# Performance work log

Measured on AMD Instinct MI355X. Metric: run time of the kernel, lower is better.

The kernel has to match this reference:

```python
import jax, jax.numpy as jnp
import numpy as np

B, L, K, D, H = 2048, 1024, 128, 64, 4


def setup_inputs() -> dict:
    key = jax.random.key(0)
    ks = jax.random.split(key, 16)
    s = 1.0 / np.sqrt(D).astype(np.float32)  # keep softmax unsaturated
    return {
        "indices": jax.random.randint(ks[0], (B, K), 0, L),
        "user_seq_emb": jax.random.normal(ks[1], (B, L, D), jnp.float32),
        "target_emb": jax.random.normal(ks[2], (B, 1, D), jnp.float32),
        "WQ": jax.random.normal(ks[3], (H, D, D), jnp.float32) * s,
        "bQ": jax.random.normal(ks[4], (H, D), jnp.float32) * s,
        "WK": jax.random.normal(ks[5], (H, D, D), jnp.float32) * s,
        "bK": jax.random.normal(ks[6], (H, D), jnp.float32) * s,
        "WV": jax.random.normal(ks[7], (H, D, D), jnp.float32) * s,
        "bV": jax.random.normal(ks[8], (H, D), jnp.float32) * s,
        "WO": jax.random.normal(ks[9], (H * D, D), jnp.float32) * s,
        "bO": jax.random.normal(ks[10], (D,), jnp.float32) * s,
        "W1": jax.random.normal(ks[11], (2 * D, D), jnp.float32) * s,
        "b1": jax.random.normal(ks[12], (D,), jnp.float32) * s,
        "W2": jax.random.normal(ks[13], (D, 1), jnp.float32) * s,
        "b2": jax.random.normal(ks[14], (1,), jnp.float32) * s,
    }


def reference(indices, user_seq_emb, target_emb, WQ, bQ, WK, bK, WV, bV,
              WO, bO, W1, b1, W2, b2):
    d = user_seq_emb.shape[-1]
    # gather top-K history items: [B, K, D]
    topk = jnp.take_along_axis(user_seq_emb, indices[:, :, None], axis=1)
    # per-head projections, vectorized over heads (original loops in Python)
    q = jnp.einsum("bod,hde->bhoe", target_emb, WQ) + bQ[None, :, None, :]  # [B,H,1,D]
    k = jnp.einsum("bkd,hde->bhke", topk, WK) + bK[None, :, None, :]        # [B,H,K,D]
    v = jnp.einsum("bkd,hde->bhke", topk, WV) + bV[None, :, None, :]        # [B,H,K,D]
    scores = jnp.einsum("bhoe,bhke->bhk", q, k) / np.sqrt(d).astype(np.float32)
    attn = jax.nn.softmax(scores, axis=-1)                                   # [B,H,K]
    heads = jnp.einsum("bhk,bhke->bhe", attn, v)                             # [B,H,D]
    mhta = heads.reshape(heads.shape[0], -1) @ WO + bO                       # [B,D]
    # prediction layer: concat with target, MLP -> logit
    x = jnp.concatenate([mhta, target_emb[:, 0, :]], axis=-1)                # [B,2D]
    h = jax.nn.relu(x @ W1 + b1)
    logit = h @ W2 + b2                                                      # [B,1]
    return logit
```

## Files before the change

### kernel.cpp

```cpp
#include <hip/hip_runtime.h>
#include <hip/hip_bf16.h>

#define BB 2048
#define LL 1024
#define KK 128
#define DD 64
#define HH 4

__global__ __launch_bounds__(256) void prep_kernel(
    const float* __restrict__ tgt, const float* __restrict__ WQ,
    const float* __restrict__ bQ, const float* __restrict__ WK,
    const float* __restrict__ bK, float* __restrict__ wkq_out,
    float* __restrict__ sb_out)
{
    __shared__ float sT[8][64];
    __shared__ float sQ[8][256];
    const int t = threadIdx.x;
    const int h = t >> 6, e = t & 63;
    const float myBQ = bQ[t];
    const float myBK = bK[t];
    for (int g = 0; g < 2; g++) {
        const int b0 = (blockIdx.x * 2 + g) * 8;
        for (int i = t; i < 512; i += 256)
            sT[i >> 6][i & 63] = tgt[(size_t)(b0 + (i >> 6)) * 64 + (i & 63)];
        __syncthreads();
        float acc[8];
        #pragma unroll
        for (int j = 0; j < 8; j++) acc[j] = myBQ;
        for (int d = 0; d < 64; d++) {
            float w = WQ[((h << 6) + d) * 64 + e];
            #pragma unroll
            for (int j = 0; j < 8; j++) acc[j] += sT[j][d] * w;
        }
        #pragma unroll
        for (int j = 0; j < 8; j++) sQ[j][t] = acc[j];
        __syncthreads();
        #pragma unroll
        for (int j = 0; j < 8; j++) {
            float p = acc[j] * myBK;
            #pragma unroll
            for (int o = 32; o > 0; o >>= 1) p += __shfl_xor(p, o);
            if (e == 0) sb_out[(b0 + j) * 4 + h] = p * 0.125f;
        }
        float acc2[8];
        #pragma unroll
        for (int j = 0; j < 8; j++) acc2[j] = 0.f;
        const float* wrow = WK + (size_t)t * 64;
        for (int i = 0; i < 64; i += 4) {
            float4 w4 = *(const float4*)(wrow + i);
            #pragma unroll
            for (int j = 0; j < 8; j++) {
                acc2[j] += w4.x * sQ[j][(h << 6) + i]
                         + w4.y * sQ[j][(h << 6) + i + 1]
                         + w4.z * sQ[j][(h << 6) + i + 2]
                         + w4.w * sQ[j][(h << 6) + i + 3];
            }
        }
        #pragma unroll
        for (int j = 0; j < 8; j++)
            wkq_out[(size_t)(b0 + j) * 256 + t] = acc2[j] * 0.125f;
        __syncthreads();
    }
}

__global__ __launch_bounds__(256) void attn_kernel(
    const int* __restrict__ idx, const float* __restrict__ seq,
    const float* __restrict__ wkq_in, const float* __restrict__ sb_in,
    float* __restrict__ ctx_out)
{
    __shared__ float sTop[KK * 65];
    __shared__ float sWkq[256];
    __shared__ float sSb[HH];
    __shared__ float sSc[HH * KK];
    __shared__ float sAt[HH * KK];
    __shared__ int sIdx[KK];
    const int t = threadIdx.x;
    const int b = blockIdx.x;
    if (t < KK) sIdx[t] = idx[b * KK + t];
    sWkq[t] = wkq_in[(size_t)b * 256 + t];
    if (t < HH) sSb[t] = sb_in[b * HH + t];
    __syncthreads();
    for (int i = t; i < 2048; i += 256) {
        int row = i >> 4, c0 = (i & 15) * 4;
        float4 v = *(const float4*)(seq + ((size_t)b * LL + sIdx[row]) * DD + c0);
        float* dst = &sTop[row * 65 + c0];
        dst[0] = v.x; dst[1] = v.y; dst[2] = v.z; dst[3] = v.w;
    }
    __syncthreads();
    #pragma unroll
    for (int s = 0; s < 2; s++) {
        int id = (s << 8) + t;
        int h = id >> 7, k = id & 127;
        float acc = 0.f;
        #pragma unroll
        for (int d = 0; d < DD; d++)
            acc += sTop[k * 65 + d] * sWkq[(h << 6) + d];
        sSc[(h << 7) + k] = acc + sSb[h];
    }
    __syncthreads();
    const int w = t >> 6, lane = t & 63;
    float x0 = sSc[(w << 7) + lane], x1 = sSc[(w << 7) + 64 + lane];
    float m = fmaxf(x0, x1);
    #pragma unroll
    for (int o = 32; o > 0; o >>= 1) m = fmaxf(m, __shfl_xor(m, o));
    float e0 = __expf(x0 - m), e1 = __expf(x1 - m);
    float s = e0 + e1;
    #pragma unroll
    for (int o = 32; o > 0; o >>= 1) s += __shfl_xor(s, o);
    float inv = 1.f / s;
    sAt[(w << 7) + lane] = e0 * inv;
    sAt[(w << 7) + 64 + lane] = e1 * inv;
    __syncthreads();
    float acc = 0.f;
    #pragma unroll 8
    for (int k = 0; k < KK; k++)
        acc += sAt[(w << 7) + k] * sTop[k * 65 + lane];
    ctx_out[(size_t)b * 256 + t] = acc;
}

__global__ __launch_bounds__(256) void out_kernel(
    const float* __restrict__ ctx_in, const float* __restrict__ tgt,
    const float* __restrict__ WV, const float* __restrict__ bV,
    const float* __restrict__ WO, const float* __restrict__ bO,
    const float* __restrict__ W1, const float* __restrict__ b1,
    const float* __restrict__ W2, const float* __restrict__ b2,
    float* __restrict__ outp)
{
    __shared__ float sCtx[8][256];
    __shared__ float sH[8][256];
    __shared__ float sP[8][256];
    __shared__ float sX[8][128];
    const int t = threadIdx.x;
    const int h = t >> 6, e = t & 63;
    const float myBV = bV[t];
    for (int g = 0; g < 2; g++) {
        const int b0 = (blockIdx.x * 2 + g) * 8;
        #pragma unroll
        for (int j = 0; j < 8; j++)
            sCtx[j][t] = ctx_in[(size_t)(b0 + j) * 256 + t];
        for (int i = t; i < 512; i += 256)
            sX[i >> 6][64 + (i & 63)] = tgt[(size_t)(b0 + (i >> 6)) * 64 + (i & 63)];
        __syncthreads();
        float acc[8];
        #pragma unroll
        for (int j = 0; j < 8; j++) acc[j] = myBV;
        for (int d = 0; d < 64; d++) {
            float w = WV[((h << 6) + d) * 64 + e];
            #pragma unroll
            for (int j = 0; j < 8; j++) acc[j] += sCtx[j][(h << 6) + d] * w;
        }
        #pragma unroll
        for (int j = 0; j < 8; j++) sH[j][t] = acc[j];
        __syncthreads();
        float pa[8];
        #pragma unroll
        for (int j = 0; j < 8; j++) pa[j] = 0.f;
        for (int i = 0; i < 64; i++) {
            float w = WO[((h << 6) + i) * 64 + e];
            #pragma unroll
            for (int j = 0; j < 8; j++) pa[j] += sH[j][(h << 6) + i] * w;
        }
        #pragma unroll
        for (int j = 0; j < 8; j++) sP[j][t] = pa[j];
        __syncthreads();
        #pragma unroll
        for (int s = 0; s < 2; s++) {
            int id = (s << 8) + t;
            int j = id >> 6, ee = id & 63;
            sX[j][ee] = sP[j][ee] + sP[j][64 + ee] + sP[j][128 + ee]
                      + sP[j][192 + ee] + bO[ee];
        }
        __syncthreads();
        #pragma unroll
        for (int s = 0; s < 2; s++) {
            int j = (s << 2) + (t >> 6);
            int n = t & 63;
            float a1 = b1[n];
            #pragma unroll 4
            for (int i = 0; i < 128; i++)
                a1 += sX[j][i] * W1[i * 64 + n];
            a1 = fmaxf(a1, 0.f);
            float p = a1 * W2[n];
            #pragma unroll
            for (int o = 32; o > 0; o >>= 1) p += __shfl_xor(p, o);
            if (n == 0) outp[b0 + j] = p + b2[0];
        }
        __syncthreads();
    }
}

extern "C" void kernel_launch(void* const* d_in, const int* in_sizes, int n_in,
                              void* d_out, int out_size, void* d_ws, size_t ws_size,
                              hipStream_t stream)
{
    const int*   idx = (const int*)d_in[0];
    const float* seq = (const float*)d_in[1];
    const float* tgt = (const float*)d_in[2];
    const float* WQ  = (const float*)d_in[3];
    const float* bQ  = (const float*)d_in[4];
    const float* WK  = (const float*)d_in[5];
    const float* bK  = (const float*)d_in[6];
    const float* WV  = (const float*)d_in[7];
    const float* bV  = (const float*)d_in[8];
    const float* WO  = (const float*)d_in[9];
    const float* bO  = (const float*)d_in[10];
    const float* W1  = (const float*)d_in[11];
    const float* b1  = (const float*)d_in[12];
    const float* W2  = (const float*)d_in[13];
    const float* b2  = (const float*)d_in[14];

    float* wkq = (float*)d_ws;
    float* sb  = wkq + (size_t)BB * 256;
    float* ctx = sb + (size_t)BB * 4;
    float* outp = (float*)d_out;

    prep_kernel<<<dim3(BB / 16), dim3(256), 0, stream>>>(tgt, WQ, bQ, WK, bK, wkq, sb);
    attn_kernel<<<dim3(BB), dim3(256), 0, stream>>>(idx, seq, wkq, sb, ctx);
    out_kernel<<<dim3(BB / 16), dim3(256), 0, stream>>>(ctx, tgt, WV, bV, WO, bO,
                                                        W1, b1, W2, b2, outp);
}
```

Baseline: 713.9 us.

## Fuse prep, attention and output MLP into one per-batch kernel

Merges the three kernels into a single kernel with one block per batch row, so the workspace round-trips for wkq, sb and ctx and two launches go away. The gather loads for the top-K rows are issued into registers before the Q/WK projection is computed, letting the gather latency overlap that math. In exchange, the weight matrices are re-read per batch row instead of being amortised over 8 rows per block, which raises L2/cache traffic and per-block serial work.

```diff
diff --git a/kernel.cpp b/kernel.cpp
--- a/kernel.cpp
+++ b/kernel.cpp
@@ -1,5 +1,4 @@
 #include <hip/hip_runtime.h>
-#include <hip/hip_bf16.h>
 
 #define BB 2048
 #define LL 1024
@@ -7,185 +6,153 @@
 #define DD 64
 #define HH 4
 
-__global__ __launch_bounds__(256) void prep_kernel(
-    const float* __restrict__ tgt, const float* __restrict__ WQ,
-    const float* __restrict__ bQ, const float* __restrict__ WK,
-    const float* __restrict__ bK, float* __restrict__ wkq_out,
-    float* __restrict__ sb_out)
-{
-    __shared__ float sT[8][64];
-    __shared__ float sQ[8][256];
-    const int t = threadIdx.x;
-    const int h = t >> 6, e = t & 63;
-    const float myBQ = bQ[t];
-    const float myBK = bK[t];
-    for (int g = 0; g < 2; g++) {
-        const int b0 = (blockIdx.x * 2 + g) * 8;
-        for (int i = t; i < 512; i += 256)
-            sT[i >> 6][i & 63] = tgt[(size_t)(b0 + (i >> 6)) * 64 + (i & 63)];
-        __syncthreads();
-        float acc[8];
-        #pragma unroll
-        for (int j = 0; j < 8; j++) acc[j] = myBQ;
-        for (int d = 0; d < 64; d++) {
-            float w = WQ[((h << 6) + d) * 64 + e];
-            #pragma unroll
-            for (int j = 0; j < 8; j++) acc[j] += sT[j][d] * w;
-        }
-        #pragma unroll
-        for (int j = 0; j < 8; j++) sQ[j][t] = acc[j];
-        __syncthreads();
-        #pragma unroll
-        for (int j = 0; j < 8; j++) {
-            float p = acc[j] * myBK;
-            #pragma unroll
-            for (int o = 32; o > 0; o >>= 1) p += __shfl_xor(p, o);
-            if (e == 0) sb_out[(b0 + j) * 4 + h] = p * 0.125f;
-        }
-        float acc2[8];
-        #pragma unroll
-        for (int j = 0; j < 8; j++) acc2[j] = 0.f;
-        const float* wrow = WK + (size_t)t * 64;
-        for (int i = 0; i < 64; i += 4) {
-            float4 w4 = *(const float4*)(wrow + i);
-            #pragma unroll
-            for (int j = 0; j < 8; j++) {
-                acc2[j] += w4.x * sQ[j][(h << 6) + i]
-                         + w4.y * sQ[j][(h << 6) + i + 1]
-                         + w4.z * sQ[j][(h << 6) + i + 2]
-                         + w4.w * sQ[j][(h << 6) + i + 3];
-            }
-        }
-        #pragma unroll
-        for (int j = 0; j < 8; j++)
-            wkq_out[(size_t)(b0 + j) * 256 + t] = acc2[j] * 0.125f;
-        __syncthreads();
-    }
-}
-
-__global__ __launch_bounds__(256) void attn_kernel(
+__global__ __launch_bounds__(256) void fused_kernel(
     const int* __restrict__ idx, const float* __restrict__ seq,
-    const float* __restrict__ wkq_in, const float* __restrict__ sb_in,
-    float* __restrict__ ctx_out)
-{
-    __shared__ float sTop[KK * 65];
-    __shared__ float sWkq[256];
-    __shared__ float sSb[HH];
-    __shared__ float sSc[HH * KK];
-    __shared__ float sAt[HH * KK];
-    __shared__ int sIdx[KK];
-    const int t = threadIdx.x;
-    const int b = blockIdx.x;
-    if (t < KK) sIdx[t] = idx[b * KK + t];
-    sWkq[t] = wkq_in[(size_t)b * 256 + t];
-    if (t < HH) sSb[t] = sb_in[b * HH + t];
-    __syncthreads();
-    for (int i = t; i < 2048; i += 256) {
-        int row = i >> 4, c0 = (i & 15) * 4;
-        float4 v = *(const float4*)(seq + ((size_t)b * LL + sIdx[row]) * DD + c0);
-        float* dst = &sTop[row * 65 + c0];
-        dst[0] = v.x; dst[1] = v.y; dst[2] = v.z; dst[3] = v.w;
-    }
-    __syncthreads();
-    #pragma unroll
-    for (int s = 0; s < 2; s++) {
-        int id = (s << 8) + t;
-        int h = id >> 7, k = id & 127;
-        float acc = 0.f;
-        #pragma unroll
-        for (int d = 0; d < DD; d++)
-            acc += sTop[k * 65 + d] * sWkq[(h << 6) + d];
-        sSc[(h << 7) + k] = acc + sSb[h];
-    }
-    __syncthreads();
-    const int w = t >> 6, lane = t & 63;
-    float x0 = sSc[(w << 7) + lane], x1 = sSc[(w << 7) + 64 + lane];
-    float m = fmaxf(x0, x1);
-    #pragma unroll
-    for (int o = 32; o > 0; o >>= 1) m = fmaxf(m, __shfl_xor(m, o));
-    float e0 = __expf(x0 - m), e1 = __expf(x1 - m);
-    float s = e0 + e1;
-    #pragma unroll
-    for (int o = 32; o > 0; o >>= 1) s += __shfl_xor(s, o);
-    float inv = 1.f / s;
-    sAt[(w << 7) + lane] = e0 * inv;
-    sAt[(w << 7) + 64 + lane] = e1 * inv;
-    __syncthreads();
-    float acc = 0.f;
-    #pragma unroll 8
-    for (int k = 0; k < KK; k++)
-        acc += sAt[(w << 7) + k] * sTop[k * 65 + lane];
-    ctx_out[(size_t)b * 256 + t] = acc;
-}
-
-__global__ __launch_bounds__(256) void out_kernel(
-    const float* __restrict__ ctx_in, const float* __restrict__ tgt,
+    const float* __restrict__ tgt,
+    const float* __restrict__ WQ, const float* __restrict__ bQ,
+    const float* __restrict__ WK, const float* __restrict__ bK,
     const float* __restrict__ WV, const float* __restrict__ bV,
     const float* __restrict__ WO, const float* __restrict__ bO,
     const float* __restrict__ W1, const float* __restrict__ b1,
     const float* __restrict__ W2, const float* __restrict__ b2,
     float* __restrict__ outp)
 {
-    __shared__ float sCtx[8][256];
-    __shared__ float sH[8][256];
-    __shared__ float sP[8][256];
-    __shared__ float sX[8][128];
+    __shared__ float sTop[KK * 65];
+    __shared__ float sT[DD];
+    __shared__ float sA[256];
+    __shared__ float sB[256];
+    __shared__ float sSc[HH * KK];
+    __shared__ float sCtx[256];
+    __shared__ float sX[2 * DD];
+    __shared__ float sSb[HH];
+
     const int t = threadIdx.x;
+    const int b = blockIdx.x;
     const int h = t >> 6, e = t & 63;
-    const float myBV = bV[t];
-    for (int g = 0; g < 2; g++) {
-        const int b0 = (blockIdx.x * 2 + g) * 8;
+    const int w = t >> 6, lane = t & 63;
+
+    const int r0 = t >> 4;
+    const int c0 = (t & 15) * 4;
+    int rows[8];
+    #pragma unroll
+    for (int j = 0; j < 8; j++) rows[j] = idx[b * KK + r0 + 16 * j];
+    float4 g[8];
+    #pragma unroll
+    for (int j = 0; j < 8; j++)
+        g[j] = *(const float4*)(seq + ((size_t)b * LL + rows[j]) * DD + c0);
+
+    if (t < DD) sT[t] = tgt[(size_t)b * DD + t];
+    __syncthreads();
+
+    float q = bQ[t];
+    #pragma unroll 8
+    for (int d = 0; d < DD; d++)
+        q += sT[d] * WQ[((h << 6) + d) * 64 + e];
+    sA[t] = q;
+
+    {
+        float p = q * bK[t];
         #pragma unroll
-        for (int j = 0; j < 8; j++)
-            sCtx[j][t] = ctx_in[(size_t)(b0 + j) * 256 + t];
-        for (int i = t; i < 512; i += 256)
-            sX[i >> 6][64 + (i & 63)] = tgt[(size_t)(b0 + (i >> 6)) * 64 + (i & 63)];
-        __syncthreads();
-        float acc[8];
+        for (int o = 32; o > 0; o >>= 1) p += __shfl_xor(p, o);
+        if (e == 0) sSb[h] = p * 0.125f;
+    }
+    __syncthreads();
+
+    {
+        float acc2 = 0.f;
+        const float* wrow = WK + (size_t)t * 64;
+        #pragma unroll 4
+        for (int i = 0; i < 64; i += 4) {
+            float4 w4 = *(const float4*)(wrow + i);
+            acc2 += w4.x * sA[(h << 6) + i]     + w4.y * sA[(h << 6) + i + 1]
+                  + w4.z * sA[(h << 6) + i + 2] + w4.w * sA[(h << 6) + i + 3];
+        }
+        sB[t] = acc2 * 0.125f;
+    }
+
+    #pragma unroll
+    for (int j = 0; j < 8; j++) {
+        float* dst = &sTop[(r0 + 16 * j) * 65 + c0];
+        dst[0] = g[j].x; dst[1] = g[j].y; dst[2] = g[j].z; dst[3] = g[j].w;
+    }
+    __syncthreads();
+
+    #pragma unroll
+    for (int s = 0; s < 2; s++) {
+        int id = (s << 8) + t;
+        int hh = id >> 7, k = id & 127;
+        float a = 0.f;
+        #pragma unroll 8
+        for (int d = 0; d < DD; d++)
+            a += sTop[k * 65 + d] * sB[(hh << 6) + d];
+        sSc[(hh << 7) + k] = a + sSb[hh];
+    }
+    __syncthreads();
+
+    {
+        float x0 = sSc[(w << 7) + lane], x1 = sSc[(w << 7) + 64 + lane];
+        float m = fmaxf(x0, x1);
         #pragma unroll
-        for (int j = 0; j < 8; j++) acc[j] = myBV;
-        for (int d = 0; d < 64; d++) {
-            float w = WV[((h << 6) + d) * 64 + e];
-            #pragma unroll
-            for (int j = 0; j < 8; j++) acc[j] += sCtx[j][(h << 6) + d] * w;
-        }
+        for (int o = 32; o > 0; o >>= 1) m = fmaxf(m, __shfl_xor(m, o));
+        float e0 = __expf(x0 - m), e1 = __expf(x1 - m);
+        float s = e0 + e1;
         #pragma unroll
-        for (int j = 0; j < 8; j++) sH[j][t] = acc[j];
-        __syncthreads();
-        float pa[8];
+        for (int o = 32; o > 0; o >>= 1) s += __shfl_xor(s, o);
+        float inv = 1.f / s;
+        sSc[(w << 7) + lane] = e0 * inv;
+        sSc[(w << 7) + 64 + lane] = e1 * inv;
+    }
+    __syncthreads();
+
+    {
+        float cacc = 0.f;
+        #pragma unroll 8
+        for (int k = 0; k < KK; k++)
+            cacc += sSc[(w << 7) + k] * sTop[k * 65 + lane];
+        sCtx[t] = cacc;
+    }
+    __syncthreads();
+
+    {
+        float hv = bV[t];
+        #pragma unroll 8
+        for (int d = 0; d < DD; d++)
+            hv += sCtx[(h << 6) + d] * WV[((h << 6) + d) * 64 + e];
+        sA[t] = hv;
+    }
+    __syncthreads();
+
+    {
+        float pa = 0.f;
+        #pragma unroll 8
+        for (int i = 0; i < 64; i++)
+            pa += sA[(h << 6) + i] * WO[((h << 6) + i) * 64 + e];
+        sB[t] = pa;
+    }
+    __syncthreads();
+
+    if (t < 64) {
+        sX[t] = sB[t] + sB[64 + t] + sB[128 + t] + sB[192 + t] + bO[t];
+        sX[64 + t] = sT[t];
+    }
+    __syncthreads();
+
+    {
+        float a1 = 0.f;
+        const int i0 = w << 5;
+        #pragma unroll 8
+        for (int i = i0; i < i0 + 32; i++)
+            a1 += sX[i] * W1[i * 64 + lane];
+        sB[(w << 6) + lane] = a1;
+    }
+    __syncthreads();
+    if (t < 64) {
+        float v = sB[t] + sB[64 + t] + sB[128 + t] + sB[192 + t] + b1[t];
+        v = fmaxf(v, 0.f);
+        float p = v * W2[t];
         #pragma unroll
-        for (int j = 0; j < 8; j++) pa[j] = 0.f;
-        for (int i = 0; i < 64; i++) {
-            float w = WO[((h << 6) + i) * 64 + e];
-            #pragma unroll
-            for (int j = 0; j < 8; j++) pa[j] += sH[j][(h << 6) + i] * w;
-        }
-        #pragma unroll
-        for (int j = 0; j < 8; j++) sP[j][t] = pa[j];
-        __syncthreads();
-        #pragma unroll
-        for (int s = 0; s < 2; s++) {
-            int id = (s << 8) + t;
-            int j = id >> 6, ee = id & 63;
-            sX[j][ee] = sP[j][ee] + sP[j][64 + ee] + sP[j][128 + ee]
-                      + sP[j][192 + ee] + bO[ee];
-        }
-        __syncthreads();
-        #pragma unroll
-        for (int s = 0; s < 2; s++) {
-            int j = (s << 2) + (t >> 6);
-            int n = t & 63;
-            float a1 = b1[n];
-            #pragma unroll 4
-            for (int i = 0; i < 128; i++)
-                a1 += sX[j][i] * W1[i * 64 + n];
-            a1 = fmaxf(a1, 0.f);
-            float p = a1 * W2[n];
-            #pragma unroll
-            for (int o = 32; o > 0; o >>= 1) p += __shfl_xor(p, o);
-            if (n == 0) outp[b0 + j] = p + b2[0];
-        }
-        __syncthreads();
+        for (int o = 32; o > 0; o >>= 1) p += __shfl_xor(p, o);
+        if (t == 0) outp[b] = p + b2[0];
     }
 }
 
@@ -208,14 +175,8 @@
     const float* b1  = (const float*)d_in[12];
     const float* W2  = (const float*)d_in[13];
     const float* b2  = (const float*)d_in[14];
-
-    float* wkq = (float*)d_ws;
-    float* sb  = wkq + (size_t)BB * 256;
-    float* ctx = sb + (size_t)BB * 4;
     float* outp = (float*)d_out;
 
-    prep_kernel<<<dim3(BB / 16), dim3(256), 0, stream>>>(tgt, WQ, bQ, WK, bK, wkq, sb);
-    attn_kernel<<<dim3(BB), dim3(256), 0, stream>>>(idx, seq, wkq, sb, ctx);
-    out_kernel<<<dim3(BB / 16), dim3(256), 0, stream>>>(ctx, tgt, WV, bV, WO, bO,
-                                                        W1, b1, W2, b2, outp);
+    fused_kernel<<<dim3(BB), dim3(256), 0, stream>>>(
+        idx, seq, tgt, WQ, bQ, WK, bK, WV, bV, WO, bO, W1, b1, W2, b2, outp);
 }
```

After: 648.6 us. -9.1%, faster.
